# Performance work log

Hardware: AMD Instinct MI355X
Metric: run time of the kernel (lower is better)

The kernel has to match this reference:

```python
import jax, jax.numpy as jnp
import numpy as np

N = 100000   # nodes
E = 1600000  # edges
IN_DIM, HID, HEADS, OUT_DIM = 8, 64, 4, 3


def _add_self_loops(src, dst, n):
    loop = jnp.arange(n, dtype=src.dtype)
    return jnp.concatenate([src, loop]), jnp.concatenate([dst, loop])


def gcn_conv(x, src, dst, n, W, b):
    # PyG GCNConv: add self-loops, symmetric normalization deg^-1/2 * deg^-1/2
    s, d = _add_self_loops(src, dst, n)
    deg = jax.ops.segment_sum(jnp.ones(s.shape[0], x.dtype), d, num_segments=n)
    dinv = jnp.where(deg > 0, jax.lax.rsqrt(deg), 0.0)
    norm = dinv[s] * dinv[d]                       # [E']
    h = x @ W                                      # [N, out]
    out = jax.ops.segment_sum(norm[:, None] * h[s], d, num_segments=n)
    return out + b


def gat_conv(x, src, dst, n, W, att_src, att_dst, b):
    # PyG GATConv, concat=True, negative_slope=0.2, self-loops added
    h = (x @ W).reshape(n, HEADS, HID)             # [N, H, C]
    s, d = _add_self_loops(src, dst, n)
    a_src = jnp.sum(h * att_src, axis=-1)          # [N, H]
    a_dst = jnp.sum(h * att_dst, axis=-1)          # [N, H]
    e = jax.nn.leaky_relu(a_src[s] + a_dst[d], negative_slope=0.2)  # [E', H]
    m = jax.lax.stop_gradient(jax.ops.segment_max(e, d, num_segments=n))
    ex = jnp.exp(e - m[d])
    denom = jax.ops.segment_sum(ex, d, num_segments=n)
    alpha = ex / (denom[d] + 1e-16)                # segment softmax over incoming edges
    out = jax.ops.segment_sum(alpha[:, :, None] * h[s], d, num_segments=n)  # [N, H, C]
    return out.reshape(n, HEADS * HID) + b


def setup_inputs() -> dict:
    key = jax.random.key(0)
    ks = jax.random.split(key, 16)
    def glorot(k, shape):
        fan = shape[0] + shape[-1]
        return jax.random.normal(k, shape, jnp.float32) * np.sqrt(2.0 / fan)
    return {
        "x": jax.random.normal(ks[0], (N, IN_DIM), jnp.float32),
        "edge_index": jax.random.randint(ks[1], (2, E), 0, N, jnp.int64 if jax.config.jax_enable_x64 else jnp.int32),
        "w1": glorot(ks[2], (IN_DIM, HID)), "b1": jnp.zeros((HID,), jnp.float32),
        "w2": glorot(ks[3], (HID, HID)),   "b2": jnp.zeros((HID,), jnp.float32),
        "w3": glorot(ks[4], (HID, HID)),   "b3": jnp.zeros((HID,), jnp.float32),
        "wg": glorot(ks[5], (HID, HEADS * HID)), "bg": jnp.zeros((HEADS * HID,), jnp.float32),
        "att_src": glorot(ks[6], (HEADS, HID)),
        "att_dst": glorot(ks[7], (HEADS, HID)),
        "wc1": glorot(ks[8], (HEADS * HID, HID)), "bc1": jnp.zeros((HID,), jnp.float32),
        "wc2": glorot(ks[9], (HID, OUT_DIM)),     "bc2": jnp.zeros((OUT_DIM,), jnp.float32),
    }


def reference(x, edge_index, w1, b1, w2, b2, w3, b3, wg, bg, att_src, att_dst, wc1, bc1, wc2, bc2):
    src, dst = edge_index[0], edge_index[1]
    n = x.shape[0]
    # stacked GCN convs with ReLU; residual when shapes match (layers 2,3)
    h = jax.nn.relu(gcn_conv(x, src, dst, n, w1, b1))
    h = h + jax.nn.relu(gcn_conv(h, src, dst, n, w2, b2))
    h = h + jax.nn.relu(gcn_conv(h, src, dst, n, w3, b3))
    # GAT attention layer (4 heads, concat)
    h_att = gat_conv(h, src, dst, n, wg, att_src, att_dst, bg)  # [N, 256]
    # classifier MLP (dropout is inference no-op)
    z = jax.nn.relu(h_att @ wc1 + bc1)
    logits = z @ wc2 + bc2
    return jax.nn.log_softmax(logits, axis=1)
```

## Files before the change

kernel.cpp:

```cpp
#include <hip/hip_runtime.h>
#include <math.h>


typedef _Float16 half8 __attribute__((ext_vector_type(8)));
typedef _Float16 f16x8 __attribute__((ext_vector_type(8)));
typedef float f32x4 __attribute__((ext_vector_type(4)));
typedef int int4v __attribute__((ext_vector_type(4)));

__device__ __forceinline__ float leaky02(float v) { return v > 0.f ? v : 0.2f * v; }


template <int CTRL>
__device__ __forceinline__ float dpp_add(float v) {
    int iv = __builtin_bit_cast(int, v);
    int r = __builtin_amdgcn_update_dpp(iv, iv, CTRL, 0xF, 0xF, false);
    return v + __builtin_bit_cast(float, r);
}
template <int OFF>
__device__ __forceinline__ float swz_add(float v) {
    int r = __builtin_amdgcn_ds_swizzle(__builtin_bit_cast(int, v), OFF);
    return v + __builtin_bit_cast(float, r);
}
template <int CTRL>
__device__ __forceinline__ float dpp_max(float v) {
    int iv = __builtin_bit_cast(int, v);
    int r = __builtin_amdgcn_update_dpp(iv, iv, CTRL, 0xF, 0xF, false);
    return fmaxf(v, __builtin_bit_cast(float, r));
}
template <int OFF>
__device__ __forceinline__ float swz_max(float v) {
    int r = __builtin_amdgcn_ds_swizzle(__builtin_bit_cast(int, v), OFF);
    return fmaxf(v, __builtin_bit_cast(float, r));
}
__device__ __forceinline__ float red8(float v) {
    v = dpp_add<0xB1>(v);
    v = dpp_add<0x4E>(v);
    v = swz_add<0x101F>(v);
    return v;
}
__device__ __forceinline__ float red16(float v) {
    v = dpp_add<0xB1>(v);
    v = dpp_add<0x4E>(v);
    v = swz_add<0x101F>(v);
    v = dpp_add<0x128>(v);
    return v;
}
__device__ __forceinline__ float red16max(float v) {
    v = dpp_max<0xB1>(v);
    v = dpp_max<0x4E>(v);
    v = swz_max<0x101F>(v);
    v = dpp_max<0x128>(v);
    return v;
}
__device__ __forceinline__ float red64(float v) {
    v = dpp_add<0xB1>(v);
    v = dpp_add<0x4E>(v);
    v = swz_add<0x101F>(v);
    v = dpp_add<0x128>(v);
    v = swz_add<0x401F>(v);
    v = v + __shfl_xor(v, 32);
    return v;
}
__device__ __forceinline__ float red32max(float v) {
    v = dpp_max<0xB1>(v);
    v = dpp_max<0x4E>(v);
    v = swz_max<0x101F>(v);
    v = dpp_max<0x128>(v);
    v = swz_max<0x401F>(v);
    return v;
}


__global__ void count_kernel(const int* __restrict__ dst, int E, int range,
                             int* __restrict__ counts) {
    int grp = blockIdx.x & 7;
    int nlo = grp * range;
    int nhi = nlo + range;
    int nblk = gridDim.x >> 3;
    int c = blockIdx.x >> 3;
    int stride4 = nblk * blockDim.x * 4;
    for (int e = (c * blockDim.x + threadIdx.x) * 4; e < E; e += stride4) {
        int4v d4;
        if (e + 3 < E) {
            d4 = *(const int4v*)(dst + e);
        } else {
#pragma unroll
            for (int j = 0; j < 4; ++j) d4[j] = (e + j < E) ? dst[e + j] : -1;
        }
#pragma unroll
        for (int j = 0; j < 4; ++j) {
            int d = d4[j];
            if (d >= nlo && d < nhi) atomicAdd(&counts[d], 1);
        }
    }
}

__global__ void scan_pass1(const int* __restrict__ counts, int n, int* __restrict__ blockSums) {
    __shared__ int sh[256];
    int base = blockIdx.x * 2048;
    int tid = threadIdx.x;
    int s = 0;
#pragma unroll
    for (int j = 0; j < 8; ++j) {
        int idx = base + tid * 8 + j;
        if (idx < n) s += counts[idx];
    }
    sh[tid] = s;
    __syncthreads();
    for (int off = 128; off > 0; off >>= 1) {
        if (tid < off) sh[tid] += sh[tid + off];
        __syncthreads();
    }
    if (tid == 0) blockSums[blockIdx.x] = sh[0];
}

__global__ void scan_pass2(const int* __restrict__ blockSums, int nb, int* __restrict__ blockOffs) {
    if (threadIdx.x == 0 && blockIdx.x == 0) {
        int run = 0;
        for (int i = 0; i < nb; ++i) { blockOffs[i] = run; run += blockSums[i]; }
    }
}

__global__ void scan_pass3(const int* __restrict__ counts, int n,
                           const int* __restrict__ blockOffs,
                           const float* __restrict__ x,
                           int* __restrict__ row_ptr, int* __restrict__ cursor,
                           float* __restrict__ dinv, float* __restrict__ rdinv,
                           _Float16* __restrict__ xs,
                           int* __restrict__ shortList, int* __restrict__ longList,
                           int* __restrict__ nodeCnts) {
    __shared__ int sh[256];
    __shared__ int shp[256];
    __shared__ int baseS, baseL;
    int base = blockIdx.x * 2048;
    int tid = threadIdx.x;
    int cnt[8];
    int local = 0;
#pragma unroll
    for (int j = 0; j < 8; ++j) {
        int idx = base + tid * 8 + j;
        cnt[j] = (idx < n) ? counts[idx] : 0;
        local += cnt[j];
    }
    sh[tid] = local;
    __syncthreads();
    for (int off = 1; off < 256; off <<= 1) {
        int v = (tid >= off) ? sh[tid - off] : 0;
        __syncthreads();
        sh[tid] += v;
        __syncthreads();
    }
    int run = blockOffs[blockIdx.x] + sh[tid] - local;
#pragma unroll
    for (int j = 0; j < 8; ++j) {
        int idx = base + tid * 8 + j;
        if (idx < n) {
            row_ptr[idx] = run;
            cursor[idx] = run;
            float dv = rsqrtf((float)(cnt[j] + 1));
            dinv[idx] = dv;
            rdinv[idx] = sqrtf((float)(cnt[j] + 1));
#pragma unroll
            for (int t = 0; t < 8; ++t) xs[idx * 8 + t] = (_Float16)(dv * x[idx * 8 + t]);
            run += cnt[j];
            if (idx == n - 1) row_ptr[n] = run;
        }
    }
    int myS = 0, myL = 0;
#pragma unroll
    for (int j = 0; j < 8; ++j) {
        int idx = base + tid * 8 + j;
        if (idx < n) { if (cnt[j] <= 15) ++myS; else ++myL; }
    }
    shp[tid] = myS | (myL << 16);
    __syncthreads();
    for (int off = 1; off < 256; off <<= 1) {
        int v = (tid >= off) ? shp[tid - off] : 0;
        __syncthreads();
        shp[tid] += v;
        __syncthreads();
    }
    if (tid == 255) {
        baseS = atomicAdd(&nodeCnts[0], shp[255] & 0xFFFF);
        baseL = atomicAdd(&nodeCnts[1], shp[255] >> 16);
    }
    __syncthreads();
    int pS = baseS + (shp[tid] & 0xFFFF) - myS;
    int pL = baseL + (shp[tid] >> 16) - myL;
#pragma unroll
    for (int j = 0; j < 8; ++j) {
        int idx = base + tid * 8 + j;
        if (idx < n) {
            if (cnt[j] <= 15) shortList[pS++] = idx;
            else              longList[pL++] = idx;
        }
    }
}

__global__ void scatter_kernel(const int* __restrict__ src, const int* __restrict__ dst,
                               int E, int range,
                               int* __restrict__ cursor, int* __restrict__ col_src) {
    int grp = blockIdx.x & 7;
    int nlo = grp * range;
    int nhi = nlo + range;
    int nblk = gridDim.x >> 3;
    int c = blockIdx.x >> 3;
    int stride4 = nblk * blockDim.x * 4;
    for (int e = (c * blockDim.x + threadIdx.x) * 4; e < E; e += stride4) {
        int4v d4, s4;
        if (e + 3 < E) {
            d4 = *(const int4v*)(dst + e);
            s4 = *(const int4v*)(src + e);
        } else {
#pragma unroll
            for (int j = 0; j < 4; ++j) {
                d4[j] = (e + j < E) ? dst[e + j] : -1;
                s4[j] = (e + j < E) ? src[e + j] : 0;
            }
        }
#pragma unroll
        for (int j = 0; j < 4; ++j) {
            int d = d4[j];
            if (d >= nlo && d < nhi) {
                int pos = atomicAdd(&cursor[d], 1);
                col_src[pos] = s4[j];
            }
        }
    }
}


__global__ void ccomb_kernel(const float* __restrict__ Wg, const float* __restrict__ bg,
                             const float* __restrict__ wc1, const float* __restrict__ bc1,
                             const float* __restrict__ att_src, const float* __restrict__ att_dst,
                             const float* __restrict__ w2, const float* __restrict__ w3,
                             _Float16* __restrict__ CcombP, float* __restrict__ bcomb,
                             float* __restrict__ wse, float* __restrict__ wde,
                             _Float16* __restrict__ W2P, _Float16* __restrict__ W3P) {
    int bid = blockIdx.x;
    int j = threadIdx.x;
    if (bid < 256) {
        int i = bid;
        float s = 0.f;
        for (int c = 0; c < 64; ++c)
            s += Wg[(i & 63) * 256 + (i >> 6) * 64 + c] * wc1[((i >> 6) * 64 + c) * 64 + j];
        _Float16 hi = (_Float16)s;
        _Float16 lo = (_Float16)(s - (float)hi);
        int kt = i >> 5, l = (((i >> 3) & 3) << 4) | (j & 15), e = i & 7, ct = j >> 4;
        CcombP[(ct * 8 + kt) * 512 + l * 8 + e] = hi;
        CcombP[(32 + ct * 8 + kt) * 512 + l * 8 + e] = lo;
    } else if (bid == 256) {
        float s = bc1[j];
        for (int i = 0; i < 256; ++i) s += bg[i] * wc1[i * 64 + j];
        bcomb[j] = s;
#pragma unroll
        for (int h = 0; h < 4; ++h) {
            float ss = 0.f, sd = 0.f;
            for (int c = 0; c < 64; ++c) {
                float w = Wg[j * 256 + h * 64 + c];
                ss += w * att_src[h * 64 + c];
                sd += w * att_dst[h * 64 + c];
            }
            wse[j * 4 + h] = ss;
            wde[j * 4 + h] = sd;
        }
    } else {
        int i = (bid < 321) ? (bid - 257) : (bid - 321);
        const float* W = (bid < 321) ? w2 : w3;
        _Float16* WP = (bid < 321) ? W2P : W3P;
        float s = W[i * 64 + j];
        _Float16 hi = (_Float16)s;
        _Float16 lo = (_Float16)(s - (float)hi);
        int kt = i >> 5, l = (((i >> 3) & 3) << 4) | (j & 15), e = i & 7, ct = j >> 4;
        WP[(ct * 2 + kt) * 512 + l * 8 + e] = hi;
        WP[(8 + ct * 2 + kt) * 512 + l * 8 + e] = lo;
    }
}


__global__ void gcn_layer1(const half8* __restrict__ xs8,
                           const float* __restrict__ W1, const float* __restrict__ b1,
                           const int* __restrict__ row_ptr, const int* __restrict__ col_src,
                           const float* __restrict__ dinv, int n,
                           _Float16* __restrict__ hs1) {
    int tid = threadIdx.x, lane = tid & 63, wid = tid >> 6;
    int node = blockIdx.x * 4 + wid;
    if (node >= n) return;
    int beg = row_ptr[node], end = row_ptr[node + 1];
    int deg = end - beg;
    float acc[8] = {0.f, 0.f, 0.f, 0.f, 0.f, 0.f, 0.f, 0.f};
    for (int base = 0; base < deg; base += 64) {
        int cs = col_src[min(beg + base + lane, end - 1)];
        half8 v = xs8[cs];
        if (base + lane < deg) {
#pragma unroll
            for (int c = 0; c < 8; ++c) acc[c] += (float)v[c];
        }
    }
#pragma unroll
    for (int c = 0; c < 8; ++c) acc[c] = red64(acc[c]);
    half8 sv = xs8[node];
    float di = dinv[node];
    float agg[8];
#pragma unroll
    for (int c = 0; c < 8; ++c) agg[c] = (acc[c] + (float)sv[c]) * di;
    float sum = b1[lane];
#pragma unroll
    for (int k = 0; k < 8; ++k) sum = fmaf(agg[k], W1[k * 64 + lane], sum);
    hs1[node * 64 + lane] = (_Float16)(di * fmaxf(sum, 0.f));
}


__global__ void gcn_agg(const _Float16* __restrict__ hs_in,
                        const int* __restrict__ row_ptr, const int* __restrict__ col_src,
                        const float* __restrict__ dinv, int n,
                        _Float16* __restrict__ aggout) {
    int tid = threadIdx.x, lane = tid & 63, wid = tid >> 6;
    int node = blockIdx.x * 4 + wid;
    if (node >= n) return;
    int t = lane >> 3, g = lane & 7;
    const half8* hs8 = (const half8*)hs_in;
    int beg = row_ptr[node], end = row_ptr[node + 1];
    int deg = end - beg;
    half8 sv = hs8[node * 8 + t];
    float ac[8];
#pragma unroll
    for (int c = 0; c < 8; ++c) ac[c] = (g == 0) ? (float)sv[c] : 0.f;
    for (int base = 0; base < deg; base += 64) {
        int cs = col_src[min(beg + base + lane, end - 1)];
        int lim = min(deg - base, 64);
        auto bodyF = [&](int eo8) {
            int s = __shfl(cs, eo8 + g);
            half8 v = hs8[s * 8 + t];
#pragma unroll
            for (int c = 0; c < 8; ++c) ac[c] += (float)v[c];
        };
        auto bodyG = [&](int eo8) {
            int eo = eo8 + g;
            int s = __shfl(cs, eo);
            half8 v = hs8[s * 8 + t];
            if (eo < lim) {
#pragma unroll
                for (int c = 0; c < 8; ++c) ac[c] += (float)v[c];
            }
        };
        int eo8 = 0;
        for (; eo8 + 16 <= lim; eo8 += 16) { bodyF(eo8); bodyF(eo8 + 8); }
        if (eo8 < lim) {
            bodyG(eo8);
            eo8 += 8;
            if (eo8 < lim) bodyG(eo8);
        }
    }
    float di = dinv[node];
#pragma unroll
    for (int c = 0; c < 8; ++c) ac[c] = red8(ac[c]) * di;
    if (g == 0) {
        half8 hv;
#pragma unroll
        for (int c = 0; c < 8; ++c) hv[c] = (_Float16)ac[c];
        *(half8*)(aggout + (size_t)node * 64 + t * 8) = hv;
    }
}


template <bool LAST>
__global__ __launch_bounds__(256) void gcn_mfma(
        const _Float16* __restrict__ agg,
        const _Float16* __restrict__ WP,
        const float* __restrict__ b,
        const _Float16* __restrict__ hs_in,
        const float* __restrict__ dinv, const float* __restrict__ rdinv,
        const float* __restrict__ wse, const float* __restrict__ wde,
        int n, _Float16* __restrict__ hout,
        float4* __restrict__ a_src4, float4* __restrict__ a_dst4) {
    __shared__ float partS[4][16][4];
    __shared__ float partD[4][16][4];
    int tid = threadIdx.x;
    int lane = tid & 63;
    int w = __builtin_amdgcn_readfirstlane(tid >> 6);
    int c16 = lane & 15, hi = lane >> 4;

    f16x8 bh[2], blo[2];
#pragma unroll
    for (int kt = 0; kt < 2; ++kt) {
        bh[kt]  = *(const f16x8*)(WP + (size_t)(w * 2 + kt) * 512 + lane * 8);
        blo[kt] = *(const f16x8*)(WP + (size_t)(8 + w * 2 + kt) * 512 + lane * 8);
    }
    int col = w * 16 + c16;
    float bl = b[col];
    float4 wev, wdv;
    if (LAST) {
        wev = ((const float4*)wse)[col];
        wdv = ((const float4*)wde)[col];
    }

    int ntiles = (n + 15) >> 4;
    for (int tile = blockIdx.x; tile < ntiles; tile += gridDim.x) {
        int rowb = tile * 16;
        int arow = min(rowb + c16, n - 1);
        const _Float16* ap = agg + (size_t)arow * 64 + hi * 8;
        f16x8 a0 = *(const f16x8*)(ap);
        f16x8 a1 = *(const f16x8*)(ap + 32);
        f32x4 acc = {0.f, 0.f, 0.f, 0.f};
        acc = __builtin_amdgcn_mfma_f32_16x16x32_f16(a0, bh[0],  acc, 0, 0, 0);
        acc = __builtin_amdgcn_mfma_f32_16x16x32_f16(a0, blo[0], acc, 0, 0, 0);
        acc = __builtin_amdgcn_mfma_f32_16x16x32_f16(a1, bh[1],  acc, 0, 0, 0);
        acc = __builtin_amdgcn_mfma_f32_16x16x32_f16(a1, blo[1], acc, 0, 0, 0);
#pragma unroll
        for (int r = 0; r < 4; ++r) {
            int noder = rowb + hi * 4 + r;
            bool ok = noder < n;
            int ni = min(noder, n - 1);
            float hp = rdinv[ni] * (float)hs_in[(size_t)ni * 64 + col];
            float z = fmaxf(acc[r] + bl, 0.f);
            float hv = hp + z;
            if (!LAST) {
                if (ok) hout[(size_t)ni * 64 + col] = (_Float16)(dinv[ni] * hv);
            } else {
                if (ok) hout[(size_t)ni * 64 + col] = (_Float16)hv;
                float s0 = red16(hv * wev.x), s1 = red16(hv * wev.y);
                float s2 = red16(hv * wev.z), s3 = red16(hv * wev.w);
                float d0 = red16(hv * wdv.x), d1 = red16(hv * wdv.y);
                float d2 = red16(hv * wdv.z), d3 = red16(hv * wdv.w);
                if (c16 == 0) {
                    *(float4*)&partS[w][hi * 4 + r][0] = make_float4(s0, s1, s2, s3);
                    *(float4*)&partD[w][hi * 4 + r][0] = make_float4(d0, d1, d2, d3);
                }
            }
        }
        if (LAST) {
            __syncthreads();
            if (tid < 16) {
                int node = rowb + tid;
                if (node < n) {
                    float4 s = make_float4(
                        partS[0][tid][0] + partS[1][tid][0] + partS[2][tid][0] + partS[3][tid][0],
                        partS[0][tid][1] + partS[1][tid][1] + partS[2][tid][1] + partS[3][tid][1],
                        partS[0][tid][2] + partS[1][tid][2] + partS[2][tid][2] + partS[3][tid][2],
                        partS[0][tid][3] + partS[1][tid][3] + partS[2][tid][3] + partS[3][tid][3]);
                    float4 d = make_float4(
                        partD[0][tid][0] + partD[1][tid][0] + partD[2][tid][0] + partD[3][tid][0],
                        partD[0][tid][1] + partD[1][tid][1] + partD[2][tid][1] + partD[3][tid][1],
                        partD[0][tid][2] + partD[1][tid][2] + partD[2][tid][2] + partD[3][tid][2],
                        partD[0][tid][3] + partD[1][tid][3] + partD[2][tid][3] + partD[3][tid][3]);
                    a_src4[node] = s;
                    a_dst4[node] = d;
                }
            }
            __syncthreads();
        }
    }
}


__global__ __launch_bounds__(256, 4) void gat_agg_short(
        const _Float16* __restrict__ h3,
        const float4* __restrict__ a_src4, const float4* __restrict__ a_dst4,
        const int* __restrict__ row_ptr, const int* __restrict__ col_src,
        const int* __restrict__ shortList, const int* __restrict__ nodeCnts,
        _Float16* __restrict__ aggout) {
    __shared__ _Float16 HsAll[4][32 * 72];
    __shared__ _Float16 wATAll[4][16 * 40];
    int tid = threadIdx.x, lane = tid & 63, wid = tid >> 6;
    int nshort = nodeCnts[0];
    int i0 = (blockIdx.x * 4 + wid) * 2;
    if (i0 >= nshort) return;
    int nodeA = shortList[i0];
    int nodeB = (i0 + 1 < nshort) ? shortList[i0 + 1] : nodeA;
    _Float16* Hs = HsAll[wid];
    _Float16* wAT = wATAll[wid];

    {
        int zm = lane >> 2;
        int zc = ((zm < 8) ? 16 : 0) + (lane & 3) * 4;
#pragma unroll
        for (int j = 0; j < 4; ++j) wAT[zm * 40 + zc + j] = (_Float16)0.f;
    }

    int q = lane >> 4, m16 = lane & 15;
    int c0 = (lane & 7) * 8;
    int sl16 = lane & 15;
    int myNode = (lane < 16) ? nodeA : ((lane < 32) ? nodeB : nodeA);
    int begL = row_ptr[myNode], endL = row_ptr[myNode + 1];
    int nslL = endL - begL + 1;
    float4 adv = a_dst4[myNode];
    int eidx = max(min(begL + sl16 - 1, endL - 1), 0);
    int cs = (sl16 == 0) ? myNode : col_src[eidx];
    float4 as = a_src4[cs];
    float vm = (sl16 < nslL && lane < 32) ? 1.f : 0.f;
    float l0 = leaky02(as.x + adv.x);
    float l1 = leaky02(as.y + adv.y);
    float l2 = leaky02(as.z + adv.z);
    float l3 = leaky02(as.w + adv.w);
    float m0 = red16max(vm > 0.f ? l0 : -1e30f);
    float m1 = red16max(vm > 0.f ? l1 : -1e30f);
    float m2 = red16max(vm > 0.f ? l2 : -1e30f);
    float m3 = red16max(vm > 0.f ? l3 : -1e30f);
    float w0 = vm * __expf(fminf(l0 - m0, 10.f));
    float w1 = vm * __expf(fminf(l1 - m1, 10.f));
    float w2 = vm * __expf(fminf(l2 - m2, 10.f));
    float w3 = vm * __expf(fminf(l3 - m3, 10.f));
    if (lane < 32) {
        int rb = (lane < 16) ? 0 : 8;
        int k = lane;
        _Float16 h0 = (_Float16)w0, h1 = (_Float16)w1;
        _Float16 h2 = (_Float16)w2, h3v = (_Float16)w3;
        wAT[(rb + 0) * 40 + k] = h0;
        wAT[(rb + 1) * 40 + k] = h1;
        wAT[(rb + 2) * 40 + k] = h2;
        wAT[(rb + 3) * 40 + k] = h3v;
        wAT[(rb + 4) * 40 + k] = (_Float16)(w0 - (float)h0);
        wAT[(rb + 5) * 40 + k] = (_Float16)(w1 - (float)h1);
        wAT[(rb + 6) * 40 + k] = (_Float16)(w2 - (float)h2);
        wAT[(rb + 7) * 40 + k] = (_Float16)(w3 - (float)h3v);
    }
#pragma unroll
    for (int i = 0; i < 4; ++i) {
        int r = i * 8 + (lane >> 3);
        int s = __shfl(cs, r);
        half8 hv = *(const half8*)(h3 + (size_t)s * 64 + c0);
        *(half8*)(Hs + r * 72 + (c0 ^ (i << 4))) = hv;
    }
    __asm__ volatile("s_waitcnt lgkmcnt(0)" ::: "memory");
    f16x8 A = *(const f16x8*)(wAT + m16 * 40 + q * 8);
    int swz = q << 4;
    const _Float16* Bb0 = Hs + (size_t)q * 8 * 72 + ((0 * 16 + m16) ^ swz);
    const _Float16* Bb1 = Hs + (size_t)q * 8 * 72 + ((1 * 16 + m16) ^ swz);
    const _Float16* Bb2 = Hs + (size_t)q * 8 * 72 + ((2 * 16 + m16) ^ swz);
    const _Float16* Bb3 = Hs + (size_t)q * 8 * 72 + ((3 * 16 + m16) ^ swz);
    f16x8 B0, B1, B2, B3;
#pragma unroll
    for (int e = 0; e < 8; ++e) {
        B0[e] = Bb0[e * 72];
        B1[e] = Bb1[e * 72];
        B2[e] = Bb2[e * 72];
        B3[e] = Bb3[e * 72];
    }
    f16x8 ONES;
#pragma unroll
    for (int e = 0; e < 8; ++e) ONES[e] = (_Float16)1.f;
    f32x4 acc0 = {0.f,0.f,0.f,0.f}, acc1 = {0.f,0.f,0.f,0.f};
    f32x4 acc2 = {0.f,0.f,0.f,0.f}, acc3 = {0.f,0.f,0.f,0.f};
    f32x4 accD = {0.f,0.f,0.f,0.f};
    acc0 = __builtin_amdgcn_mfma_f32_16x16x32_f16(A, B0, acc0, 0, 0, 0);
    acc1 = __builtin_amdgcn_mfma_f32_16x16x32_f16(A, B1, acc1, 0, 0, 0);
    acc2 = __builtin_amdgcn_mfma_f32_16x16x32_f16(A, B2, acc2, 0, 0, 0);
    acc3 = __builtin_amdgcn_mfma_f32_16x16x32_f16(A, B3, acc3, 0, 0, 0);
    accD = __builtin_amdgcn_mfma_f32_16x16x32_f16(A, ONES, accD, 0, 0, 0);

    float tot[4][4], rdv[4];
#pragma unroll
    for (int r = 0; r < 4; ++r) {
        tot[0][r] = acc0[r] + __shfl_xor(acc0[r], 16);
        tot[1][r] = acc1[r] + __shfl_xor(acc1[r], 16);
        tot[2][r] = acc2[r] + __shfl_xor(acc2[r], 16);
        tot[3][r] = acc3[r] + __shfl_xor(acc3[r], 16);
        float d = accD[r] + __shfl_xor(accD[r], 16);
        rdv[r] = 1.f / (d + 1e-16f);
    }
    int outNode = -1;
    if (lane < 16) outNode = nodeA;
    else if (lane >= 32 && lane < 48 && nodeB != nodeA) outNode = nodeB;
    if (outNode >= 0) {
        size_t ob = (size_t)outNode * 256 + (lane & 15);
#pragma unroll
        for (int r = 0; r < 4; ++r) {
#pragma unroll
            for (int ct = 0; ct < 4; ++ct)
                aggout[ob + r * 64 + ct * 16] = (_Float16)(tot[ct][r] * rdv[r]);
        }
    }
}


__global__ __launch_bounds__(256, 4) void gat_agg_long(
        const _Float16* __restrict__ h3,
        const float4* __restrict__ a_src4, const float4* __restrict__ a_dst4,
        const int* __restrict__ row_ptr, const int* __restrict__ col_src,
        const int* __restrict__ longList, const int* __restrict__ nodeCnts,
        _Float16* __restrict__ aggout) {
    __shared__ _Float16 HsAll[4][32 * 72];
    __shared__ _Float16 wATAll[4][16 * 40];
    int tid = threadIdx.x, lane = tid & 63, wid = tid >> 6;
    int nlong = nodeCnts[1];
    int li = blockIdx.x * 4 + wid;
    if (li >= nlong) return;
    int node = longList[li];
    _Float16* Hs = HsAll[wid];
    _Float16* wAT = wATAll[wid];

    int q = lane >> 4, m16 = lane & 15;
    float4 ad = a_dst4[node];
    int beg = row_ptr[node], end = row_ptr[node + 1];
    int deg = end - beg;
    int nslots = deg + 1;
    int c0 = (lane & 7) * 8;

    int swz = q << 4;
    const _Float16* Bb0 = Hs + (size_t)q * 8 * 72 + ((0 * 16 + m16) ^ swz);
    const _Float16* Bb1 = Hs + (size_t)q * 8 * 72 + ((1 * 16 + m16) ^ swz);
    const _Float16* Bb2 = Hs + (size_t)q * 8 * 72 + ((2 * 16 + m16) ^ swz);
    const _Float16* Bb3 = Hs + (size_t)q * 8 * 72 + ((3 * 16 + m16) ^ swz);
    const f16x8* Ab = (const f16x8*)(wAT + m16 * 40 + q * 8);
    f16x8 ONES;
#pragma unroll
    for (int e = 0; e < 8; ++e) ONES[e] = (_Float16)1.f;

    f32x4 acc0 = {0.f,0.f,0.f,0.f}, acc1 = {0.f,0.f,0.f,0.f};
    f32x4 acc2 = {0.f,0.f,0.f,0.f}, acc3 = {0.f,0.f,0.f,0.f};
    f32x4 accD = {0.f,0.f,0.f,0.f};
    float m0 = 0.f, m1 = 0.f, m2 = 0.f, m3 = 0.f;

    for (int base = 0; base < nslots; base += 32) {
        int sl = base + (lane & 31);
        int eidx = max(min(beg + sl - 1, end - 1), 0);
        int cs = (sl == 0) ? node : col_src[eidx];
        float4 as = a_src4[cs];
        float vm = (sl < nslots && lane < 32) ? 1.f : 0.f;
        float l0 = leaky02(as.x + ad.x);
        float l1 = leaky02(as.y + ad.y);
        float l2 = leaky02(as.z + ad.z);
        float l3 = leaky02(as.w + ad.w);
        if (base == 0) {
            m0 = red32max(vm > 0.f ? l0 : -1e30f);
            m1 = red32max(vm > 0.f ? l1 : -1e30f);
            m2 = red32max(vm > 0.f ? l2 : -1e30f);
            m3 = red32max(vm > 0.f ? l3 : -1e30f);
        }
        float w0 = vm * __expf(fminf(l0 - m0, 10.f));
        float w1 = vm * __expf(fminf(l1 - m1, 10.f));
        float w2 = vm * __expf(fminf(l2 - m2, 10.f));
        float w3 = vm * __expf(fminf(l3 - m3, 10.f));
        if (lane < 32) {
            int s32 = lane & 31;
            _Float16 h0 = (_Float16)w0, h1 = (_Float16)w1;
            _Float16 h2 = (_Float16)w2, h3v = (_Float16)w3;
            wAT[0 * 40 + s32] = h0;
            wAT[1 * 40 + s32] = h1;
            wAT[2 * 40 + s32] = h2;
            wAT[3 * 40 + s32] = h3v;
            wAT[4 * 40 + s32] = (_Float16)(w0 - (float)h0);
            wAT[5 * 40 + s32] = (_Float16)(w1 - (float)h1);
            wAT[6 * 40 + s32] = (_Float16)(w2 - (float)h2);
            wAT[7 * 40 + s32] = (_Float16)(w3 - (float)h3v);
        }
#pragma unroll
        for (int i = 0; i < 4; ++i) {
            int r = i * 8 + (lane >> 3);
            int s = __shfl(cs, r);
            half8 hv = *(const half8*)(h3 + (size_t)s * 64 + c0);
            *(half8*)(Hs + r * 72 + (c0 ^ (i << 4))) = hv;
        }
        __asm__ volatile("s_waitcnt lgkmcnt(0)" ::: "memory");
        f16x8 A = *Ab;
        f16x8 B0, B1, B2, B3;
#pragma unroll
        for (int e = 0; e < 8; ++e) {
            B0[e] = Bb0[e * 72];
            B1[e] = Bb1[e * 72];
            B2[e] = Bb2[e * 72];
            B3[e] = Bb3[e * 72];
        }
        acc0 = __builtin_amdgcn_mfma_f32_16x16x32_f16(A, B0, acc0, 0, 0, 0);
        acc1 = __builtin_amdgcn_mfma_f32_16x16x32_f16(A, B1, acc1, 0, 0, 0);
        acc2 = __builtin_amdgcn_mfma_f32_16x16x32_f16(A, B2, acc2, 0, 0, 0);
        acc3 = __builtin_amdgcn_mfma_f32_16x16x32_f16(A, B3, acc3, 0, 0, 0);
        accD = __builtin_amdgcn_mfma_f32_16x16x32_f16(A, ONES, accD, 0, 0, 0);
        __asm__ volatile("s_waitcnt lgkmcnt(0)" ::: "memory");
    }

    float tot[4][4], rdv[4];
#pragma unroll
    for (int r = 0; r < 4; ++r) {
        tot[0][r] = acc0[r] + __shfl_xor(acc0[r], 16);
        tot[1][r] = acc1[r] + __shfl_xor(acc1[r], 16);
        tot[2][r] = acc2[r] + __shfl_xor(acc2[r], 16);
        tot[3][r] = acc3[r] + __shfl_xor(acc3[r], 16);
        float d = accD[r] + __shfl_xor(accD[r], 16);
        rdv[r] = 1.f / (d + 1e-16f);
    }
    if (lane < 16) {
        size_t ob = (size_t)node * 256 + lane;
#pragma unroll
        for (int r = 0; r < 4; ++r) {
#pragma unroll
            for (int ct = 0; ct < 4; ++ct)
                aggout[ob + r * 64 + ct * 16] = (_Float16)(tot[ct][r] * rdv[r]);
        }
    }
}


__global__ __launch_bounds__(256) void mlp_mfma(
        const _Float16* __restrict__ agg,
        const _Float16* __restrict__ CP,
        const float* __restrict__ bcomb,
        const float* __restrict__ wc2, const float* __restrict__ bc2,
        int n, float* __restrict__ out) {
    __shared__ float part[4][16][3];
    int tid = threadIdx.x;
    int lane = tid & 63;
    int w = __builtin_amdgcn_readfirstlane(tid >> 6);
    int c16 = lane & 15, hi = lane >> 4;

    f16x8 bh[8], blo[8];
#pragma unroll
    for (int kt = 0; kt < 8; ++kt) {
        bh[kt]  = *(const f16x8*)(CP + (size_t)(w * 8 + kt) * 512 + lane * 8);
        blo[kt] = *(const f16x8*)(CP + (size_t)(32 + w * 8 + kt) * 512 + lane * 8);
    }
    int col = w * 16 + c16;
    float bc  = bcomb[col];
    float w20 = wc2[col * 3 + 0], w21 = wc2[col * 3 + 1], w22 = wc2[col * 3 + 2];
    float bb0 = bc2[0], bb1 = bc2[1], bb2 = bc2[2];

    int ntiles = (n + 15) >> 4;
    for (int tile = blockIdx.x; tile < ntiles; tile += gridDim.x) {
        int rowb = tile * 16;
        int row = min(rowb + c16, n - 1);
        const _Float16* ap = agg + (size_t)row * 256 + hi * 8;
        f16x8 a[8];
#pragma unroll
        for (int kt = 0; kt < 8; ++kt) a[kt] = *(const f16x8*)(ap + kt * 32);
        f32x4 acc = {0.f, 0.f, 0.f, 0.f};
#pragma unroll
        for (int kt = 0; kt < 8; ++kt) {
            acc = __builtin_amdgcn_mfma_f32_16x16x32_f16(a[kt], bh[kt],  acc, 0, 0, 0);
            acc = __builtin_amdgcn_mfma_f32_16x16x32_f16(a[kt], blo[kt], acc, 0, 0, 0);
        }
        float pr[4][3];
#pragma unroll
        for (int r = 0; r < 4; ++r) {
            float z = fmaxf(acc[r] + bc, 0.f);
            pr[r][0] = red16(z * w20);
            pr[r][1] = red16(z * w21);
            pr[r][2] = red16(z * w22);
        }
        if (c16 == 0) {
#pragma unroll
            for (int r = 0; r < 4; ++r) {
                part[w][hi * 4 + r][0] = pr[r][0];
                part[w][hi * 4 + r][1] = pr[r][1];
                part[w][hi * 4 + r][2] = pr[r][2];
            }
        }
        __syncthreads();
        if (tid < 16) {
            int node = rowb + tid;
            if (node < n) {
                float e0 = part[0][tid][0] + part[1][tid][0] + part[2][tid][0] + part[3][tid][0] + bb0;
                float e1 = part[0][tid][1] + part[1][tid][1] + part[2][tid][1] + part[3][tid][1] + bb1;
                float e2 = part[0][tid][2] + part[1][tid][2] + part[2][tid][2] + part[3][tid][2] + bb2;
                float mx = fmaxf(e0, fmaxf(e1, e2));
                float lse = mx + logf(expf(e0 - mx) + expf(e1 - mx) + expf(e2 - mx));
                out[(size_t)node * 3 + 0] = e0 - lse;
                out[(size_t)node * 3 + 1] = e1 - lse;
                out[(size_t)node * 3 + 2] = e2 - lse;
            }
        }
        __syncthreads();
    }
}


extern "C" void kernel_launch(void* const* d_in, const int* in_sizes, int n_in,
                              void* d_out, int out_size, void* d_ws, size_t ws_size,
                              hipStream_t stream) {
    const float* x       = (const float*)d_in[0];
    const int*   ei      = (const int*)d_in[1];
    const float* w1      = (const float*)d_in[2];
    const float* b1      = (const float*)d_in[3];
    const float* w2      = (const float*)d_in[4];
    const float* b2      = (const float*)d_in[5];
    const float* w3      = (const float*)d_in[6];
    const float* b3      = (const float*)d_in[7];
    const float* wg      = (const float*)d_in[8];
    const float* bg      = (const float*)d_in[9];
    const float* att_s   = (const float*)d_in[10];
    const float* att_d   = (const float*)d_in[11];
    const float* wc1     = (const float*)d_in[12];
    const float* bc1     = (const float*)d_in[13];
    const float* wc2     = (const float*)d_in[14];
    const float* bc2     = (const float*)d_in[15];
    float* out = (float*)d_out;

    const int N = in_sizes[0] / 8;
    const int E = in_sizes[1] / 2;
    const int* srcv = ei;
    const int* dstv = ei + E;

    char* ws = (char*)d_ws;
    size_t off = 0;
    auto alloc = [&](size_t bytes) -> char* {
        char* p = ws + off;
        off += (bytes + 255) & ~(size_t)255;
        return p;
    };
    int*      counts    = (int*)alloc((size_t)N * 4);
    int*      row_ptr   = (int*)alloc((size_t)(N + 1) * 4);
    int*      cursor    = (int*)alloc((size_t)N * 4);
    int*      col_src   = (int*)alloc((size_t)E * 4);
    int*      blockSums = (int*)alloc(4096 * 4);
    int*      blockOffs = (int*)alloc(4096 * 4);
    float*    dinv      = (float*)alloc((size_t)N * 4);
    float*    rdinv     = (float*)alloc((size_t)N * 4);
    _Float16* xs        = (_Float16*)alloc((size_t)N * 8 * 2);
    float*    a_src     = (float*)alloc((size_t)N * 16);
    float*    a_dst     = (float*)alloc((size_t)N * 16);
    float*    wse       = (float*)alloc(256 * 4);
    float*    wde       = (float*)alloc(256 * 4);
    _Float16* CcombP    = (_Float16*)alloc(64 * 1024);
    float*    bcomb     = (float*)alloc(64 * 4);
    _Float16* W2P       = (_Float16*)alloc(16 * 1024);
    _Float16* W3P       = (_Float16*)alloc(16 * 1024);
    int*      shortList = (int*)alloc((size_t)N * 4);
    int*      longList  = (int*)alloc((size_t)N * 4);
    int*      nodeCnts  = (int*)alloc(256);
    _Float16* bufA      = (_Float16*)alloc((size_t)N * 64 * 2);
    _Float16* bufB      = (_Float16*)alloc((size_t)N * 64 * 2);
    _Float16* aggbuf    = (_Float16*)alloc((size_t)N * 256 * 2);
    _Float16* hs1 = bufA;
    _Float16* hs2 = bufB;
    _Float16* h3  = bufA;
    _Float16* aggA = aggbuf;
    (void)ws_size; (void)n_in; (void)out_size;

    hipMemsetAsync(counts, 0, (size_t)N * 4, stream);
    hipMemsetAsync(nodeCnts, 0, 8, stream);

    const int TPB = 256;
    int range = (N + 7) / 8;
    count_kernel<<<1024, TPB, 0, stream>>>(dstv, E, range, counts);

    int NB = (N + 2047) / 2048;
    scan_pass1<<<NB, TPB, 0, stream>>>(counts, N, blockSums);
    scan_pass2<<<1, 64, 0, stream>>>(blockSums, NB, blockOffs);
    scan_pass3<<<NB, TPB, 0, stream>>>(counts, N, blockOffs, x,
                                       row_ptr, cursor, dinv, rdinv, xs,
                                       shortList, longList, nodeCnts);
    scatter_kernel<<<2048, TPB, 0, stream>>>(srcv, dstv, E, range, cursor, col_src);

    ccomb_kernel<<<385, 64, 0, stream>>>(wg, bg, wc1, bc1, att_s, att_d, w2, w3,
                                         CcombP, bcomb, wse, wde, W2P, W3P);

    int gridN = (N + 3) / 4;
    gcn_layer1<<<gridN, TPB, 0, stream>>>((const half8*)xs, w1, b1, row_ptr, col_src,
                                          dinv, N, hs1);

    gcn_agg<<<gridN, TPB, 0, stream>>>(hs1, row_ptr, col_src, dinv, N, aggA);
    gcn_mfma<false><<<2048, TPB, 0, stream>>>(aggA, W2P, b2, hs1, dinv, rdinv,
                                              nullptr, nullptr, N, hs2,
                                              nullptr, nullptr);
    gcn_agg<<<gridN, TPB, 0, stream>>>(hs2, row_ptr, col_src, dinv, N, aggA);
    gcn_mfma<true><<<2048, TPB, 0, stream>>>(aggA, W3P, b3, hs2, dinv, rdinv,
                                             wse, wde, N, h3,
                                             (float4*)a_src, (float4*)a_dst);

    int gridS = ((N + 1) / 2 + 3) / 4;
    gat_agg_short<<<gridS, TPB, 0, stream>>>(h3, (const float4*)a_src,
                                             (const float4*)a_dst, row_ptr, col_src,
                                             shortList, nodeCnts, aggbuf);
    gat_agg_long<<<gridN, TPB, 0, stream>>>(h3, (const float4*)a_src,
                                            (const float4*)a_dst, row_ptr, col_src,
                                            longList, nodeCnts, aggbuf);
    mlp_mfma<<<2048, TPB, 0, stream>>>(aggbuf, CcombP, bcomb, wc2, bc2, N, out);
}
```

Before: 519.1 us.

## Pre-bucketize edges by destination range before count and scatter passes

Adds a bucketize kernel that partitions edges into 8 destination-range buckets, using an LDS prefix scan and a staging buffer so global writes are coalesced. The count and scatter kernels then read only their own bucket instead of scanning the full edge list with a range filter, which removes the 8x redundant reads of dst/src. In exchange it adds an extra pass that writes and re-reads about 2E ints, reuses the aggregation buffer as scratch, and relies on a fixed bucket capacity (BCAP) that assumes roughly uniform destinations.

```diff
diff --git a/kernel.cpp b/kernel.cpp
--- a/kernel.cpp
+++ b/kernel.cpp
@@ -6,6 +6,8 @@
 typedef _Float16 f16x8 __attribute__((ext_vector_type(8)));
 typedef float f32x4 __attribute__((ext_vector_type(4)));
 typedef int int4v __attribute__((ext_vector_type(4)));
+
+#define BCAP 210000
 
 __device__ __forceinline__ float leaky02(float v) { return v > 0.f ? v : 0.2f * v; }
 
@@ -71,26 +73,115 @@
 }
 
 
-__global__ void count_kernel(const int* __restrict__ dst, int E, int range,
-                             int* __restrict__ counts) {
+__global__ __launch_bounds__(256) void bucketize(
+        const int* __restrict__ src, const int* __restrict__ dst,
+        int E, int range,
+        int* __restrict__ bucketCur, int* __restrict__ bSrc, int* __restrict__ bDst) {
+    __shared__ unsigned sScan[4][256];
+    __shared__ unsigned long long sPair[2048];
+    __shared__ int sBase[8];
+    __shared__ int sLds[9];
+    int tid = threadIdx.x;
+    int e0 = blockIdx.x * 2048 + tid * 8;
+
+    int d[8], s[8], rr[8];
+    bool ok[8];
+    if (e0 + 7 < E) {
+        int4v da = *(const int4v*)(dst + e0);
+        int4v db = *(const int4v*)(dst + e0 + 4);
+        int4v sa = *(const int4v*)(src + e0);
+        int4v sb = *(const int4v*)(src + e0 + 4);
+#pragma unroll
+        for (int j = 0; j < 4; ++j) { d[j] = da[j]; d[j + 4] = db[j]; s[j] = sa[j]; s[j + 4] = sb[j]; ok[j] = true; ok[j + 4] = true; }
+    } else {
+#pragma unroll
+        for (int j = 0; j < 8; ++j) {
+            ok[j] = (e0 + j < E);
+            d[j] = ok[j] ? dst[e0 + j] : 0;
+            s[j] = ok[j] ? src[e0 + j] : 0;
+        }
+    }
+    unsigned hcnt = 0;
+#pragma unroll
+    for (int j = 0; j < 8; ++j) {
+        int r = min(d[j] / range, 7);
+        rr[j] = r;
+        if (ok[j]) hcnt += 1u << (r * 4);
+    }
+#pragma unroll
+    for (int k = 0; k < 4; ++k)
+        sScan[k][tid] = ((hcnt >> (k * 8)) & 0xF) | (((hcnt >> (k * 8 + 4)) & 0xF) << 16);
+    __syncthreads();
+    for (int off = 1; off < 256; off <<= 1) {
+        unsigned v0 = (tid >= off) ? sScan[0][tid - off] : 0;
+        unsigned v1 = (tid >= off) ? sScan[1][tid - off] : 0;
+        unsigned v2 = (tid >= off) ? sScan[2][tid - off] : 0;
+        unsigned v3 = (tid >= off) ? sScan[3][tid - off] : 0;
+        __syncthreads();
+        sScan[0][tid] += v0; sScan[1][tid] += v1; sScan[2][tid] += v2; sScan[3][tid] += v3;
+        __syncthreads();
+    }
+    if (tid < 8) {
+        int k = tid >> 1, sh = (tid & 1) * 16;
+        int tot = (sScan[k][255] >> sh) & 0xFFFF;
+        sBase[tid] = atomicAdd(&bucketCur[tid], tot);
+    }
+    if (tid == 0) {
+        int run = 0;
+#pragma unroll
+        for (int r = 0; r < 8; ++r) {
+            sLds[r] = run;
+            run += (sScan[r >> 1][255] >> ((r & 1) * 16)) & 0xFFFF;
+        }
+        sLds[8] = run;
+    }
+    __syncthreads();
+    unsigned placed = 0;
+#pragma unroll
+    for (int j = 0; j < 8; ++j) {
+        if (ok[j]) {
+            int r = rr[j];
+            int k = r >> 1, sh = (r & 1) * 16;
+            int incl = (sScan[k][tid] >> sh) & 0xFFFF;
+            int mine = (hcnt >> (r * 4)) & 0xF;
+            int ex = incl - mine;
+            int pc = (placed >> (r * 4)) & 0xF;
+            placed += 1u << (r * 4);
+            sPair[sLds[r] + ex + pc] =
+                ((unsigned long long)(unsigned)d[j] << 32) | (unsigned)s[j];
+        }
+    }
+    __syncthreads();
+    int btotal = sLds[8];
+    for (int i = tid; i < btotal; i += 256) {
+        unsigned long long p = sPair[i];
+        int r = 0;
+#pragma unroll
+        for (int k = 1; k < 8; ++k) r += (i >= sLds[k]);
+        size_t g = (size_t)r * BCAP + sBase[r] + (i - sLds[r]);
+        bSrc[g] = (int)(unsigned)(p & 0xFFFFFFFFu);
+        bDst[g] = (int)(unsigned)(p >> 32);
+    }
+}
+
+__global__ void count_b(const int* __restrict__ bDst,
+                        const int* __restrict__ bucketCur,
+                        int* __restrict__ counts) {
     int grp = blockIdx.x & 7;
-    int nlo = grp * range;
-    int nhi = nlo + range;
+    int cnt = bucketCur[grp];
+    const int* bd = bDst + (size_t)grp * BCAP;
     int nblk = gridDim.x >> 3;
     int c = blockIdx.x >> 3;
     int stride4 = nblk * blockDim.x * 4;
-    for (int e = (c * blockDim.x + threadIdx.x) * 4; e < E; e += stride4) {
-        int4v d4;
-        if (e + 3 < E) {
-            d4 = *(const int4v*)(dst + e);
+    for (int e = (c * blockDim.x + threadIdx.x) * 4; e < cnt; e += stride4) {
+        if (e + 3 < cnt) {
+            int4v d4 = *(const int4v*)(bd + e);
+#pragma unroll
+            for (int j = 0; j < 4; ++j) atomicAdd(&counts[d4[j]], 1);
         } else {
 #pragma unroll
-            for (int j = 0; j < 4; ++j) d4[j] = (e + j < E) ? dst[e + j] : -1;
-        }
-#pragma unroll
-        for (int j = 0; j < 4; ++j) {
-            int d = d4[j];
-            if (d >= nlo && d < nhi) atomicAdd(&counts[d], 1);
+            for (int j = 0; j < 4; ++j)
+                if (e + j < cnt) atomicAdd(&counts[bd[e + j]], 1);
         }
     }
 }
@@ -197,33 +288,32 @@
     }
 }
 
-__global__ void scatter_kernel(const int* __restrict__ src, const int* __restrict__ dst,
-                               int E, int range,
-                               int* __restrict__ cursor, int* __restrict__ col_src) {
+__global__ void scatter_b(const int* __restrict__ bSrc, const int* __restrict__ bDst,
+                          const int* __restrict__ bucketCur,
+                          int* __restrict__ cursor, int* __restrict__ col_src) {
     int grp = blockIdx.x & 7;
-    int nlo = grp * range;
-    int nhi = nlo + range;
+    int cnt = bucketCur[grp];
+    const int* bd = bDst + (size_t)grp * BCAP;
+    const int* bs = bSrc + (size_t)grp * BCAP;
     int nblk = gridDim.x >> 3;
     int c = blockIdx.x >> 3;
     int stride4 = nblk * blockDim.x * 4;
-    for (int e = (c * blockDim.x + threadIdx.x) * 4; e < E; e += stride4) {
-        int4v d4, s4;
-        if (e + 3 < E) {
-            d4 = *(const int4v*)(dst + e);
-            s4 = *(const int4v*)(src + e);
+    for (int e = (c * blockDim.x + threadIdx.x) * 4; e < cnt; e += stride4) {
+        if (e + 3 < cnt) {
+            int4v d4 = *(const int4v*)(bd + e);
+            int4v s4 = *(const int4v*)(bs + e);
+#pragma unroll
+            for (int j = 0; j < 4; ++j) {
+                int pos = atomicAdd(&cursor[d4[j]], 1);
+                col_src[pos] = s4[j];
+            }
         } else {
 #pragma unroll
             for (int j = 0; j < 4; ++j) {
-                d4[j] = (e + j < E) ? dst[e + j] : -1;
-                s4[j] = (e + j < E) ? src[e + j] : 0;
-            }
-        }
-#pragma unroll
-        for (int j = 0; j < 4; ++j) {
-            int d = d4[j];
-            if (d >= nlo && d < nhi) {
-                int pos = atomicAdd(&cursor[d], 1);
-                col_src[pos] = s4[j];
+                if (e + j < cnt) {
+                    int pos = atomicAdd(&cursor[bd[e + j]], 1);
+                    col_src[pos] = bs[e + j];
+                }
             }
         }
     }
@@ -817,6 +907,7 @@
     int*      shortList = (int*)alloc((size_t)N * 4);
     int*      longList  = (int*)alloc((size_t)N * 4);
     int*      nodeCnts  = (int*)alloc(256);
+    int*      bucketCur = (int*)alloc(256);
     _Float16* bufA      = (_Float16*)alloc((size_t)N * 64 * 2);
     _Float16* bufB      = (_Float16*)alloc((size_t)N * 64 * 2);
     _Float16* aggbuf    = (_Float16*)alloc((size_t)N * 256 * 2);
@@ -824,14 +915,20 @@
     _Float16* hs2 = bufB;
     _Float16* h3  = bufA;
     _Float16* aggA = aggbuf;
+    int* bSrc = (int*)aggbuf;
+    int* bDst = bSrc + (size_t)8 * BCAP;
     (void)ws_size; (void)n_in; (void)out_size;
 
     hipMemsetAsync(counts, 0, (size_t)N * 4, stream);
     hipMemsetAsync(nodeCnts, 0, 8, stream);
+    hipMemsetAsync(bucketCur, 0, 32, stream);
 
     const int TPB = 256;
     int range = (N + 7) / 8;
-    count_kernel<<<1024, TPB, 0, stream>>>(dstv, E, range, counts);
+
+    int gridBk = (E + 2047) / 2048;
+    bucketize<<<gridBk, TPB, 0, stream>>>(srcv, dstv, E, range, bucketCur, bSrc, bDst);
+    count_b<<<2048, TPB, 0, stream>>>(bDst, bucketCur, counts);
 
     int NB = (N + 2047) / 2048;
     scan_pass1<<<NB, TPB, 0, stream>>>(counts, N, blockSums);
@@ -839,7 +936,7 @@
     scan_pass3<<<NB, TPB, 0, stream>>>(counts, N, blockOffs, x,
                                        row_ptr, cursor, dinv, rdinv, xs,
                                        shortList, longList, nodeCnts);
-    scatter_kernel<<<2048, TPB, 0, stream>>>(srcv, dstv, E, range, cursor, col_src);
+    scatter_b<<<2048, TPB, 0, stream>>>(bSrc, bDst, bucketCur, cursor, col_src);
 
     ccomb_kernel<<<385, 64, 0, stream>>>(wg, bg, wc1, bc1, att_s, att_d, w2, w3,
                                          CcombP, bcomb, wse, wde, W2P, W3P);
```

Result: slower. 530.0 us (+2.1%).
